# Performance work log

Hardware: AMD Instinct MI355X
Metric: run time of the kernel (lower is better)

The kernel has to match this reference:

```python
import jax, jax.numpy as jnp
import numpy as np

IN_DIM = 128
OUT_DIM = 128
SPLINE_ORDER = 3
GRID_SIZE = 5
NUM_BASIS = GRID_SIZE + SPLINE_ORDER  # 8


def _make_grid():
    # linspace(-1, 1, grid_size+1) extended by spline_order knots on each side
    steps = GRID_SIZE + 1
    g = np.linspace(-1.0, 1.0, steps, dtype=np.float32)
    h = (g[-1] - g[0]) / (steps - 1)
    for _ in range(SPLINE_ORDER):
        g = np.concatenate([[g[0] - h], g, [g[-1] + h]])
    # expand to [in_dim, G]
    return jnp.asarray(np.broadcast_to(g, (IN_DIM, g.shape[0])).copy())


def setup_inputs() -> dict:
    key = jax.random.key(0)
    kx, kc, kw = jax.random.split(key, 3)
    x = jax.random.normal(kx, (8192, IN_DIM), dtype=jnp.float32)
    grid = _make_grid()                                                  # [in, 12]
    spline_coeff = jax.random.normal(kc, (IN_DIM, OUT_DIM, NUM_BASIS), dtype=jnp.float32)
    base_weight = jax.random.normal(kw, (IN_DIM, OUT_DIM), dtype=jnp.float32)
    scale = jnp.ones((1,), dtype=jnp.float32)
    return {"x": x, "grid": grid, "spline_coeff": spline_coeff,
            "base_weight": base_weight, "scale": scale}


def _b_spline_basis(x, grid, order):
    # x: [B, in]; grid: [in, G] -> basis [B, in, G-1-order]
    xg = x[:, :, None]            # [B, in, 1]
    g = grid[None, :, :]          # [1, in, G]
    basis = ((xg >= g[:, :, :-1]) & (xg < g[:, :, 1:])).astype(x.dtype)
    basis = jnp.nan_to_num(basis)
    for k in range(1, order + 1):
        left = (xg - g[:, :, :-(k + 1)]) / (g[:, :, k:-1] - g[:, :, :-(k + 1)]) * basis[:, :, :-1]
        right = (g[:, :, k + 1:] - xg) / (g[:, :, k + 1:] - g[:, :, 1:-k]) * basis[:, :, 1:]
        basis = jnp.nan_to_num(left + right)
    return basis


def reference(x, grid, spline_coeff, base_weight, scale):
    silu = jax.nn.silu(x)                                   # [B, in]
    basis = _b_spline_basis(x, grid, SPLINE_ORDER)          # [B, in, num_basis]
    spline = jnp.einsum('bij,ikj->bik', basis, spline_coeff)  # [B, in, out]
    base = silu[:, :, None] * base_weight[None, :, :]       # [B, in, out]
    y = (base + spline) * scale
    return y.sum(axis=1)                                    # [B, out]
```

## Files before the change

### kernel.cpp

```cpp
#include <hip/hip_runtime.h>
#include <hip/hip_bf16.h>
#include <cstdint>
#include <cstddef>

#define IN_DIM 128
#define OUT_DIM 128
#define NB 8
#define BM 64
#define NT 9
#define A_ROW_BYTES 2304
#define A_BYTES (BM * A_ROW_BYTES)

using bf16 = __hip_bfloat16;
typedef __attribute__((ext_vector_type(8))) short short8;
typedef __attribute__((ext_vector_type(4))) float f32x4;

__device__ __forceinline__ void basis_weights(float xv, float g0, float inv_h,
                                              int& j, float& w0, float& w1,
                                              float& w2, float& w3) {
    float t = (xv - g0) * inv_h;
    float jf = floorf(t);
    j = (int)jf;
    float u = t - jf;
    float um = 1.f - u;
    float u2 = u * u, u3 = u2 * u;
    w0 = um * um * um * (1.f / 6.f);
    w1 = (3.f * u3 - 6.f * u2 + 4.f) * (1.f / 6.f);
    w2 = (-3.f * u3 + 3.f * u2 + 3.f * u + 1.f) * (1.f / 6.f);
    w3 = u3 * (1.f / 6.f);
}

__device__ __forceinline__ unsigned short to_bf16_bits(float v) {
    bf16 h = __float2bfloat16(v);
    return *(unsigned short*)&h;
}

__device__ __forceinline__ short8 pack8(const float4& a, const float4& b) {
    short8 p;
    p[0] = (short)to_bf16_bits(a.x); p[1] = (short)to_bf16_bits(a.y);
    p[2] = (short)to_bf16_bits(a.z); p[3] = (short)to_bf16_bits(a.w);
    p[4] = (short)to_bf16_bits(b.x); p[5] = (short)to_bf16_bits(b.y);
    p[6] = (short)to_bf16_bits(b.z); p[7] = (short)to_bf16_bits(b.w);
    return p;
}

__global__ __launch_bounds__(1024)
void k_kan(const float* __restrict__ x, const float* __restrict__ grid,
           const float* __restrict__ C, const float* __restrict__ W,
           const float* __restrict__ scale, float* __restrict__ out) {
    __shared__ __align__(16) char smem[A_BYTES];

    const int tid = threadIdx.x;
    const int lane = tid & 63;
    const int m0 = blockIdx.x * BM;
    const int wave = tid >> 6;
    const int w = wave & 3;
    const int g = wave >> 2;
    const int r0 = lane & 15;
    const int ksub = lane >> 4;

    int ocol[2];
    ocol[0] = w * 32 + r0;
    ocol[1] = w * 32 + 16 + r0;

    float4 cb[2][2];
    float4 pf[2][2];

    auto load_spline = [&](int t, float4 (&dst)[2][2]) {
        int i = t * 16 + g * 4 + ksub;
#pragma unroll
        for (int n = 0; n < 2; ++n) {
            const float* src = C + ((size_t)i * 128 + ocol[n]) * 8;
            dst[n][0] = *(const float4*)src;
            dst[n][1] = *(const float4*)(src + 4);
        }
    };
    auto load_base = [&](float4 (&dst)[2][2]) {
        int ibase = (g * 4 + ksub) * 8;
#pragma unroll
        for (int n = 0; n < 2; ++n) {
            float v[8];
#pragma unroll
            for (int e = 0; e < 8; ++e)
                v[e] = W[(size_t)(ibase + e) * 128 + ocol[n]];
            dst[n][0] = make_float4(v[0], v[1], v[2], v[3]);
            dst[n][1] = make_float4(v[4], v[5], v[6], v[7]);
        }
    };

    load_spline(0, cb);

    {
        int row = tid >> 4, ip = tid & 15;
        const float* xr = x + (size_t)(m0 + row) * IN_DIM + ip * 8;
        float4 xa = *(const float4*)xr;
        float4 xb = *(const float4*)(xr + 4);
        float xv[8] = {xa.x, xa.y, xa.z, xa.w, xb.x, xb.y, xb.z, xb.w};
        float g0 = grid[0];
        float inv_h = 1.f / (grid[4] - grid[3]);
        char* Arow = smem + row * A_ROW_BYTES;
        short8 sil;
#pragma unroll
        for (int e = 0; e < 8; ++e) {
            float v = xv[e];
            sil[e] = (short)to_bf16_bits(v / (1.f + __expf(-v)));
            int j; float w0, w1, w2, w3;
            basis_weights(v, g0, inv_h, j, w0, w1, w2, w3);
            bool inr = (j >= 0) && (j < 11);
            short8 bas;
#pragma unroll
            for (int m = 0; m < 8; ++m) {
                int k2 = m - (j - 3);
                float val = 0.f;
                if (inr && k2 >= 0 && k2 < 4)
                    val = (k2 == 0) ? w0 : (k2 == 1) ? w1 : (k2 == 2) ? w2 : w3;
                bas[m] = (short)to_bf16_bits(val);
            }
            int chunk = (ip * 8 + e) ^ (row & 7);
            *(short8*)(Arow + chunk * 16) = bas;
        }
        int chunk = (128 + ip) ^ (row & 7);
        *(short8*)(Arow + chunk * 16) = sil;
    }
    __syncthreads();

    f32x4 acc[4][2];
#pragma unroll
    for (int rg = 0; rg < 4; ++rg)
#pragma unroll
        for (int n = 0; n < 2; ++n) acc[rg][n] = 0.f;

#pragma unroll
    for (int t = 0; t < NT; ++t) {
        if (t + 1 < 8)        load_spline(t + 1, pf);
        else if (t + 1 == 8)  load_base(pf);

        short8 b[2];
#pragma unroll
        for (int n = 0; n < 2; ++n)
            b[n] = pack8(cb[n][0], cb[n][1]);

        const int c = t * 16 + g * 4 + ksub;
        short8 a[4];
#pragma unroll
        for (int rg = 0; rg < 4; ++rg) {
            int row = rg * 16 + r0;
            int cs = c ^ (row & 7);
            a[rg] = *(const short8*)(smem + row * A_ROW_BYTES + cs * 16);
        }
#pragma unroll
        for (int rg = 0; rg < 4; ++rg)
#pragma unroll
            for (int n = 0; n < 2; ++n)
                acc[rg][n] = __builtin_amdgcn_mfma_f32_16x16x32_bf16(
                    a[rg], b[n], acc[rg][n], 0, 0, 0);

        if (t + 1 < NT) {
#pragma unroll
            for (int n = 0; n < 2; ++n)
#pragma unroll
                for (int h = 0; h < 2; ++h)
                    cb[n][h] = pf[n][h];
        }
    }

    __syncthreads();
    float* pane = (float*)smem;
    if (g > 0) {
        const int pbase = (w * 3 + (g - 1)) * (64 * 33);
#pragma unroll
        for (int rg = 0; rg < 4; ++rg)
#pragma unroll
            for (int n = 0; n < 2; ++n)
#pragma unroll
                for (int q = 0; q < 4; ++q) {
                    int row = rg * 16 + ksub * 4 + q;
                    pane[pbase + row * 33 + n * 16 + r0] = acc[rg][n][q];
                }
    }
    __syncthreads();
    if (g == 0) {
        float s = scale[0];
        const int pb0 = (w * 3 + 0) * (64 * 33);
        const int pb1 = (w * 3 + 1) * (64 * 33);
        const int pb2 = (w * 3 + 2) * (64 * 33);
#pragma unroll
        for (int rg = 0; rg < 4; ++rg)
#pragma unroll
            for (int n = 0; n < 2; ++n)
#pragma unroll
                for (int q = 0; q < 4; ++q) {
                    int row = rg * 16 + ksub * 4 + q;
                    int po = row * 33 + n * 16 + r0;
                    float v = acc[rg][n][q] + pane[pb0 + po] + pane[pb1 + po] + pane[pb2 + po];
                    out[(size_t)(m0 + row) * OUT_DIM + w * 32 + n * 16 + r0] = v * s;
                }
    }
}

__global__ void k_naive(const float* __restrict__ x, const float* __restrict__ grid,
                        const float* __restrict__ C, const float* __restrict__ W,
                        const float* __restrict__ scale, float* __restrict__ out) {
    __shared__ float sS[128];
    __shared__ float sB[128][8];
    int b = blockIdx.x, t = threadIdx.x;
    float xv = x[(size_t)b * IN_DIM + t];
    float g0 = grid[0];
    float inv_h = 1.f / (grid[4] - grid[3]);
    sS[t] = xv / (1.f + __expf(-xv));
    int j; float w0, w1, w2, w3;
    basis_weights(xv, g0, inv_h, j, w0, w1, w2, w3);
    bool inrange = (j >= 0) && (j < 11);
#pragma unroll
    for (int m = 0; m < 8; ++m) {
        int k2 = m - (j - 3);
        float val = 0.f;
        if (inrange && k2 >= 0 && k2 < 4)
            val = (k2 == 0) ? w0 : (k2 == 1) ? w1 : (k2 == 2) ? w2 : w3;
        sB[t][m] = val;
    }
    __syncthreads();
    float acc = 0.f;
    for (int i = 0; i < IN_DIM; ++i) {
        acc += sS[i] * W[(size_t)i * OUT_DIM + t];
        const float* c = C + ((size_t)i * OUT_DIM + t) * NB;
#pragma unroll
        for (int m = 0; m < 8; ++m) acc += sB[i][m] * c[m];
    }
    out[(size_t)b * OUT_DIM + t] = acc * scale[0];
}

extern "C" void kernel_launch(void* const* d_in, const int* in_sizes, int n_in,
                              void* d_out, int out_size, void* d_ws, size_t ws_size,
                              hipStream_t stream) {
    const float* x     = (const float*)d_in[0];
    const float* grid  = (const float*)d_in[1];
    const float* C     = (const float*)d_in[2];
    const float* W     = (const float*)d_in[3];
    const float* scale = (const float*)d_in[4];
    float* out = (float*)d_out;

    int B = in_sizes[0] / IN_DIM;

    if ((B % BM) == 0) {
        k_kan<<<B / BM, 1024, 0, stream>>>(x, grid, C, W, scale, out);
    } else {
        k_naive<<<B, 128, 0, stream>>>(x, grid, C, W, scale, out);
    }
}
```

Measured before the change: 18.67 us.

## Split output columns across blocks and double-buffer per-step feature generation

The kernel now launches twice as many 512-thread blocks, each covering 64 output columns. The B-spline and SiLU features are no longer built up front for all inputs; each K-step computes its slice into a double-buffered LDS tile while the MFMAs for the previous slice run, which shrinks LDS use and is meant to overlap feature math with compute. The trade-off is that each x row's feature transform is now done twice, once per column half, and every step adds a barrier.

Result: no change. 18.98 us (+1.6%).

```diff
diff --git a/kernel.cpp b/kernel.cpp
--- a/kernel.cpp
+++ b/kernel.cpp
@@ -7,9 +7,11 @@
 #define OUT_DIM 128
 #define NB 8
 #define BM 64
+#define BN 64
 #define NT 9
-#define A_ROW_BYTES 2304
-#define A_BYTES (BM * A_ROW_BYTES)
+#define BUFB (64 * 256)
+#define PANE_F (64 * 33)
+#define SMEM_BYTES (6 * PANE_F * 4)
 
 using bf16 = __hip_bfloat16;
 typedef __attribute__((ext_vector_type(8))) short short8;
@@ -44,28 +46,34 @@
     return p;
 }
 
-__global__ __launch_bounds__(1024)
+__global__ __launch_bounds__(512)
 void k_kan(const float* __restrict__ x, const float* __restrict__ grid,
            const float* __restrict__ C, const float* __restrict__ W,
            const float* __restrict__ scale, float* __restrict__ out) {
-    __shared__ __align__(16) char smem[A_BYTES];
+    __shared__ __align__(16) char smem[SMEM_BYTES];
 
     const int tid = threadIdx.x;
     const int lane = tid & 63;
-    const int m0 = blockIdx.x * BM;
     const int wave = tid >> 6;
-    const int w = wave & 3;
-    const int g = wave >> 2;
+    const int g = wave >> 1;
+    const int w = wave & 1;
+    const int m0 = (blockIdx.x >> 1) * BM;
+    const int n0 = (blockIdx.x & 1) * BN;
     const int r0 = lane & 15;
     const int ksub = lane >> 4;
 
     int ocol[2];
-    ocol[0] = w * 32 + r0;
-    ocol[1] = w * 32 + 16 + r0;
-
-    float4 cb[2][2];
-    float4 pf[2][2];
-
+    ocol[0] = n0 + w * 32 + r0;
+    ocol[1] = n0 + w * 32 + 16 + r0;
+
+    const float g0v = grid[0];
+    const float inv_h = 1.f / (grid[4] - grid[3]);
+
+    const int frow = tid >> 3;
+    const int fih = tid & 7;
+    char* const Arow_base = smem + frow * 256;
+
+    float4 cb[2][2], pf[2][2];
     auto load_spline = [&](int t, float4 (&dst)[2][2]) {
         int i = t * 16 + g * 4 + ksub;
 #pragma unroll
@@ -88,24 +96,13 @@
         }
     };
 
-    load_spline(0, cb);
-
-    {
-        int row = tid >> 4, ip = tid & 15;
-        const float* xr = x + (size_t)(m0 + row) * IN_DIM + ip * 8;
-        float4 xa = *(const float4*)xr;
-        float4 xb = *(const float4*)(xr + 4);
-        float xv[8] = {xa.x, xa.y, xa.z, xa.w, xb.x, xb.y, xb.z, xb.w};
-        float g0 = grid[0];
-        float inv_h = 1.f / (grid[4] - grid[3]);
-        char* Arow = smem + row * A_ROW_BYTES;
-        short8 sil;
-#pragma unroll
-        for (int e = 0; e < 8; ++e) {
-            float v = xv[e];
-            sil[e] = (short)to_bf16_bits(v / (1.f + __expf(-v)));
+    auto feat_spline = [&](int t, int buf) {
+        float2 xv = *(const float2*)(x + (size_t)(m0 + frow) * IN_DIM + t * 16 + fih * 2);
+        float xe[2] = {xv.x, xv.y};
+#pragma unroll
+        for (int e = 0; e < 2; ++e) {
             int j; float w0, w1, w2, w3;
-            basis_weights(v, g0, inv_h, j, w0, w1, w2, w3);
+            basis_weights(xe[e], g0v, inv_h, j, w0, w1, w2, w3);
             bool inr = (j >= 0) && (j < 11);
             short8 bas;
 #pragma unroll
@@ -116,12 +113,28 @@
                     val = (k2 == 0) ? w0 : (k2 == 1) ? w1 : (k2 == 2) ? w2 : w3;
                 bas[m] = (short)to_bf16_bits(val);
             }
-            int chunk = (ip * 8 + e) ^ (row & 7);
-            *(short8*)(Arow + chunk * 16) = bas;
-        }
-        int chunk = (128 + ip) ^ (row & 7);
-        *(short8*)(Arow + chunk * 16) = sil;
-    }
+            int ci = fih * 2 + e;
+            *(short8*)(Arow_base + buf * BUFB + ((ci ^ (frow & 7)) << 4)) = bas;
+        }
+    };
+    auto feat_base = [&](int buf) {
+#pragma unroll
+        for (int e = 0; e < 2; ++e) {
+            int ci = fih * 2 + e;
+            const float* xr = x + (size_t)(m0 + frow) * IN_DIM + ci * 8;
+            float4 xa = *(const float4*)xr;
+            float4 xb = *(const float4*)(xr + 4);
+            float xv[8] = {xa.x, xa.y, xa.z, xa.w, xb.x, xb.y, xb.z, xb.w};
+            short8 sil;
+#pragma unroll
+            for (int q = 0; q < 8; ++q)
+                sil[q] = (short)to_bf16_bits(xv[q] / (1.f + __expf(-xv[q])));
+            *(short8*)(Arow_base + buf * BUFB + ((ci ^ (frow & 7)) << 4)) = sil;
+        }
+    };
+
+    load_spline(0, cb);
+    feat_spline(0, 0);
     __syncthreads();
 
     f32x4 acc[4][2];
@@ -130,23 +143,27 @@
 #pragma unroll
         for (int n = 0; n < 2; ++n) acc[rg][n] = 0.f;
 
+    int cur = 0;
 #pragma unroll
     for (int t = 0; t < NT; ++t) {
         if (t + 1 < 8)        load_spline(t + 1, pf);
         else if (t + 1 == 8)  load_base(pf);
 
+        if (t + 1 < 8)        feat_spline(t + 1, cur ^ 1);
+        else if (t + 1 == 8)  feat_base(cur ^ 1);
+
         short8 b[2];
 #pragma unroll
         for (int n = 0; n < 2; ++n)
             b[n] = pack8(cb[n][0], cb[n][1]);
 
-        const int c = t * 16 + g * 4 + ksub;
+        const int c = g * 4 + ksub;
         short8 a[4];
 #pragma unroll
         for (int rg = 0; rg < 4; ++rg) {
             int row = rg * 16 + r0;
             int cs = c ^ (row & 7);
-            a[rg] = *(const short8*)(smem + row * A_ROW_BYTES + cs * 16);
+            a[rg] = *(const short8*)(smem + cur * BUFB + row * 256 + cs * 16);
         }
 #pragma unroll
         for (int rg = 0; rg < 4; ++rg)
@@ -162,12 +179,13 @@
                 for (int h = 0; h < 2; ++h)
                     cb[n][h] = pf[n][h];
         }
-    }
-
-    __syncthreads();
+        __syncthreads();
+        cur ^= 1;
+    }
+
     float* pane = (float*)smem;
     if (g > 0) {
-        const int pbase = (w * 3 + (g - 1)) * (64 * 33);
+        const int pbase = (w * 3 + (g - 1)) * PANE_F;
 #pragma unroll
         for (int rg = 0; rg < 4; ++rg)
 #pragma unroll
@@ -181,9 +199,9 @@
     __syncthreads();
     if (g == 0) {
         float s = scale[0];
-        const int pb0 = (w * 3 + 0) * (64 * 33);
-        const int pb1 = (w * 3 + 1) * (64 * 33);
-        const int pb2 = (w * 3 + 2) * (64 * 33);
+        const int pb0 = (w * 3 + 0) * PANE_F;
+        const int pb1 = (w * 3 + 1) * PANE_F;
+        const int pb2 = (w * 3 + 2) * PANE_F;
 #pragma unroll
         for (int rg = 0; rg < 4; ++rg)
 #pragma unroll
@@ -193,7 +211,7 @@
                     int row = rg * 16 + ksub * 4 + q;
                     int po = row * 33 + n * 16 + r0;
                     float v = acc[rg][n][q] + pane[pb0 + po] + pane[pb1 + po] + pane[pb2 + po];
-                    out[(size_t)(m0 + row) * OUT_DIM + w * 32 + n * 16 + r0] = v * s;
+                    out[(size_t)(m0 + row) * OUT_DIM + n0 + w * 32 + n * 16 + r0] = v * s;
                 }
     }
 }
@@ -243,7 +261,7 @@
     int B = in_sizes[0] / IN_DIM;
 
     if ((B % BM) == 0) {
-        k_kan<<<B / BM, 1024, 0, stream>>>(x, grid, C, W, scale, out);
+        k_kan<<<(B / BM) * 2, 512, 0, stream>>>(x, grid, C, W, scale, out);
     } else {
         k_naive<<<B, 128, 0, stream>>>(x, grid, C, W, scale, out);
     }
```
